# Kernel tuning notes

Measured on AMD Instinct MI355X. Metric: run time of the kernel, lower is better.

Reference implementation:

```python
import jax, jax.numpy as jnp
import numpy as np

V, E, U, B, T = 32000, 512, 1024, 32, 256


def setup_inputs() -> dict:
    key = jax.random.key(0)
    ks = jax.random.split(key, 6)
    rn = lambda k, shp, sc: jax.random.normal(k, shp, dtype=jnp.float32) * sc
    return {
        "x": jax.random.randint(ks[0], (B, T), 0, V, dtype=jnp.int32),
        "emb": rn(ks[1], (V, E), 0.02),
        "W_f": rn(ks[2], (E, 3 * U), 0.02),
        "U_f": rn(ks[3], (U, 3 * U), 0.02),
        "b_f": jnp.zeros((2, 3 * U), jnp.float32),
        "W_b": rn(ks[4], (E, 3 * U), 0.02),
        "U_b": rn(ks[5], (U, 3 * U), 0.02),
        "b_b": jnp.zeros((2, 3 * U), jnp.float32),
        "h0_f": jnp.zeros((B, U), jnp.float32),
        "h0_b": jnp.zeros((B, U), jnp.float32),
    }


def _gru_dir(x_tbe, h0, W, Ur, b):
    """Keras GRUCell (reset_after=True) over time. x_tbe: [T,B,E]."""
    # Precompute all input projections at once: [T,B,3U]
    xW = jnp.einsum('tbe,eg->tbg', x_tbe, W) + b[0]

    def step(h, xw):
        hU = h @ Ur + b[1]                      # [B,3U]
        xz, xr, xh = jnp.split(xw, 3, axis=-1)
        hz, hr, hn = jnp.split(hU, 3, axis=-1)
        z = jax.nn.sigmoid(xz + hz)
        r = jax.nn.sigmoid(xr + hr)
        n = jnp.tanh(xh + r * hn)
        h_new = z * h + (1.0 - z) * n
        return h_new, h_new

    hT, ys = jax.lax.scan(step, h0, xW)
    return ys, hT                                # ys: [T,B,U]


def reference(x, emb, W_f, U_f, b_f, W_b, U_b, b_b, h0_f, h0_b):
    xe = emb[x]                                  # [B,T,E] embedding lookup
    xt = jnp.transpose(xe, (1, 0, 2))            # [T,B,E]
    y_f, h_f = _gru_dir(xt, h0_f, W_f, U_f, b_f)
    y_b, h_b = _gru_dir(xt[::-1], h0_b, W_b, U_b, b_b)
    y_b = y_b[::-1]                              # re-align backward outputs in time
    y = jnp.concatenate([y_f, y_b], axis=-1)     # [T,B,2U]
    y = jnp.transpose(y, (1, 0, 2))              # [B,T,2U]
    return (y, h_f, h_b)
```

## Files before the change

kernel.cpp:

```cpp
#include <hip/hip_runtime.h>
#include <hip/hip_bf16.h>


typedef __attribute__((ext_vector_type(8))) short bf16x8;
typedef __attribute__((ext_vector_type(4))) float f32x4;

__device__ __forceinline__ f32x4 mfma_bf16(bf16x8 a, bf16x8 b, f32x4 c) {
  return __builtin_amdgcn_mfma_f32_16x16x32_bf16(a, b, c, 0, 0, 0);
}

__device__ __forceinline__ bf16x8 ld_b128(const __hip_bfloat16* p) {
  bf16x8 r; asm volatile("global_load_dwordx4 %0, %1, off" : "=v"(r) : "v"(p)); return r;
}
__device__ __forceinline__ bf16x8 ld_b128_dev(const unsigned* p) {
  bf16x8 r; asm volatile("global_load_dwordx4 %0, %1, off sc0 sc1" : "=v"(r) : "v"(p)); return r;
}
__device__ __forceinline__ unsigned ld_u32_pl(const void* p) {
  unsigned r; asm volatile("global_load_dword %0, %1, off" : "=v"(r) : "v"(p)); return r;
}
__device__ __forceinline__ unsigned ld_u32_dev(const unsigned* p) {
  unsigned r; asm volatile("global_load_dword %0, %1, off sc0 sc1" : "=v"(r) : "v"(p)); return r;
}
__device__ __forceinline__ void st_u32_dev(unsigned* p, unsigned v) {
  asm volatile("global_store_dword %0, %1, off sc0 sc1" :: "v"(p), "v"(v) : "memory");
}

__device__ __forceinline__ float bfsel(unsigned wd, int hi) {
  return __uint_as_float(hi ? (wd & 0xFFFF0000u) : (wd << 16));
}
__device__ __forceinline__ unsigned bfbits(float x) {
  return (unsigned)__builtin_bit_cast(unsigned short, __float2bfloat16(x));
}

#define WAITV(N) asm volatile("s_waitcnt vmcnt(" #N ")" ::: "memory")
#define SB0() __builtin_amdgcn_sched_barrier(0)


__global__ __launch_bounds__(256) void transpose_cast(const float* __restrict__ src,
                                                      __hip_bfloat16* __restrict__ dst,
                                                      int R, int C) {
  __shared__ float tile[32][33];
  const int tid = threadIdx.x;
  const int bc = blockIdx.x * 32;
  const int br = blockIdx.y * 32;
#pragma unroll
  for (int i = 0; i < 4; ++i) {
    int idx = tid + i * 256;
    int r = idx >> 5, c = idx & 31;
    tile[r][c] = src[(size_t)(br + r) * C + bc + c];
  }
  __syncthreads();
#pragma unroll
  for (int i = 0; i < 4; ++i) {
    int idx = tid + i * 256;
    int r = idx >> 5, c = idx & 31;
    dst[(size_t)(bc + r) * R + br + c] = __float2bfloat16(tile[c][r]);
  }
}

__global__ __launch_bounds__(256) void gather_embed(const int* __restrict__ x,
                                                    const float* __restrict__ emb,
                                                    __hip_bfloat16* __restrict__ A) {
  int ch = blockIdx.x * 256 + threadIdx.x;
  int row = ch >> 6, seg = ch & 63;
  int b = row & 31, t = row >> 5;
  int idx = x[b * 256 + t];
  const float* s = emb + (size_t)idx * 512 + seg * 8;
  float4 f0 = *(const float4*)(s);
  float4 f1 = *(const float4*)(s + 4);
  __hip_bfloat16 h[8];
  h[0] = __float2bfloat16(f0.x); h[1] = __float2bfloat16(f0.y);
  h[2] = __float2bfloat16(f0.z); h[3] = __float2bfloat16(f0.w);
  h[4] = __float2bfloat16(f1.x); h[5] = __float2bfloat16(f1.y);
  h[6] = __float2bfloat16(f1.z); h[7] = __float2bfloat16(f1.w);
  *(uint4*)(A + (size_t)row * 512 + seg * 8) = *(const uint4*)h;
}

__global__ __launch_bounds__(256) void init_h(const float* __restrict__ h0f,
                                              const float* __restrict__ h0b,
                                              unsigned* __restrict__ H,
                                              unsigned* __restrict__ FLG) {
  int i = blockIdx.x * 256 + threadIdx.x;
  int w = i >> 13, rem = i & 8191;
  int row = rem >> 9, p = rem & 511;
  const float* h0 = (w & 1) ? h0b : h0f;
  int b = (w >> 1) * 16 + row;
  float f0 = h0[b * 1024 + 2 * p];
  float f1 = h0[b * 1024 + 2 * p + 1];
  H[w * 16384 + row * 512 + p] = bfbits(f0) | (bfbits(f1) << 16);
  if (i < 8192) FLG[i] = 0u;
}

__global__ __launch_bounds__(256) void gemm_xw(const __hip_bfloat16* __restrict__ A,
                                               const __hip_bfloat16* __restrict__ B,
                                               __hip_bfloat16* __restrict__ C) {
  __shared__ char sm[2 * 128 * 80];
  const int tid = threadIdx.x;
  const int bn = blockIdx.x, bm = blockIdx.y;
  const int l = tid & 63, w = tid >> 6;
  const int wm = w & 1, wn = w >> 1;
  const int lr = l & 15, lk = l >> 4;
  f32x4 acc[4][4] = {};
  for (int k0 = 0; k0 < 512; k0 += 32) {
    __syncthreads();
#pragma unroll
    for (int i = 0; i < 2; ++i) {
      int ch = tid + i * 256;
      int row = ch >> 2, kq = ch & 3;
      uint4 va = *(const uint4*)(A + (size_t)(bm * 128 + row) * 512 + k0 + kq * 8);
      *(uint4*)(sm + row * 80 + kq * 16) = va;
      uint4 vb = *(const uint4*)(B + (size_t)(bn * 128 + row) * 512 + k0 + kq * 8);
      *(uint4*)(sm + 10240 + row * 80 + kq * 16) = vb;
    }
    __syncthreads();
    bf16x8 af[4], bfr[4];
#pragma unroll
    for (int m = 0; m < 4; ++m)
      af[m] = *(const bf16x8*)(sm + (wm * 64 + m * 16 + lr) * 80 + lk * 16);
#pragma unroll
    for (int n = 0; n < 4; ++n)
      bfr[n] = *(const bf16x8*)(sm + 10240 + (wn * 64 + n * 16 + lr) * 80 + lk * 16);
#pragma unroll
    for (int m = 0; m < 4; ++m)
#pragma unroll
      for (int n = 0; n < 4; ++n)
        acc[m][n] = mfma_bf16(af[m], bfr[n], acc[m][n]);
  }
#pragma unroll
  for (int m = 0; m < 4; ++m)
#pragma unroll
    for (int n = 0; n < 4; ++n)
#pragma unroll
      for (int v = 0; v < 4; ++v) {
        int row = bm * 128 + wm * 64 + m * 16 + lk * 4 + v;
        int col = bn * 128 + wn * 64 + n * 16 + lr;
        C[(size_t)row * 6144 + col] = __float2bfloat16(acc[m][n][v]);
      }
}

__global__ __launch_bounds__(512, 2) void gru_persist(
    const __hip_bfloat16* __restrict__ xW,
    const __hip_bfloat16* __restrict__ UT,
    const float* __restrict__ bias_f,
    const float* __restrict__ bias_b,
    const float* __restrict__ h0_f,
    const float* __restrict__ h0_b,
    unsigned* H,
    unsigned* FLG,
    float* __restrict__ out) {
  const int bi = blockIdx.x;
  const int w = bi & 3;
  const int r = bi >> 2;
  const int dir = w & 1, mh = w >> 1;
  const int tid = threadIdx.x;
  const int l = tid & 63, q = tid >> 6;
  const int lr = l & 15, lk = l >> 4;
  const int c0 = r * 32;

  __shared__ float xacc[8][6][16][20];

  bf16x8 ub[6][4];
#pragma unroll
  for (int g = 0; g < 3; ++g)
#pragma unroll
    for (int ch = 0; ch < 2; ++ch) {
      const __hip_bfloat16* Urow =
          UT + (size_t)(dir * 3072 + g * 1024 + c0 + ch * 16 + lr) * 1024 + q * 128 + lk * 8;
#pragma unroll
      for (int kc = 0; kc < 4; ++kc)
        ub[g * 2 + ch][kc] = ld_b128(Urow + kc * 32);
    }
  WAITV(0);
  SB0();

  const int crow = tid & 15;
  const int cp = tid >> 4;
  const int cb = mh * 16 + crow;
  const int cg = c0 + 2 * cp;
  float2 bz0, br0, bn0, bz1, br1, bn1, hp;
  if (tid < 256) {
    const float* bias = dir ? bias_b : bias_f;
    bz0 = *(const float2*)&bias[cg];
    br0 = *(const float2*)&bias[1024 + cg];
    bn0 = *(const float2*)&bias[2048 + cg];
    bz1 = *(const float2*)&bias[3072 + cg];
    br1 = *(const float2*)&bias[4096 + cg];
    bn1 = *(const float2*)&bias[5120 + cg];
    const float* h0 = dir ? h0_b : h0_f;
    hp = *(const float2*)&h0[(size_t)cb * 1024 + cg];
  }

  unsigned* Hw  = H + w * 16384;
  unsigned* FLw = FLG + w * 2048;
  const unsigned* flp = FLw + (16 * q + (l & 15)) * 16;
  unsigned* myflag = FLw + (r * 4 + q) * 16;

  for (int s = 0; s < 256; ++s) {
    const int par = s & 1;
    const int t = dir ? (255 - s) : s;

    unsigned xwz = 0, xwr = 0, xwn = 0;
    if (q < 4) {
      const __hip_bfloat16* xp = xW + (size_t)(t * 32 + cb) * 6144 + dir * 3072 + cg;
      xwz = ld_u32_pl(xp);
      xwr = ld_u32_pl(xp + 1024);
      xwn = ld_u32_pl(xp + 2048);
    }

    {
      const unsigned tg = (unsigned)s;
      for (;;) {
        unsigned f = ld_u32_dev(flp);
        WAITV(0);
        SB0();
        if (__all(f >= tg)) break;
        __builtin_amdgcn_s_sleep(1);
      }
    }

    const unsigned* hrow = Hw + par * 8192 + lr * 512 + q * 64 + lk * 4;
    bf16x8 hb[4];
#pragma unroll
    for (int kc = 0; kc < 4; ++kc)
      hb[kc] = ld_b128_dev(hrow + kc * 16);

    f32x4 acc[6] = {};
#define KSTEP(kc, n)                                                     \
    WAITV(n); SB0();                                                     \
    acc[0] = mfma_bf16(hb[kc], ub[0][kc], acc[0]);                       \
    acc[1] = mfma_bf16(hb[kc], ub[1][kc], acc[1]);                       \
    acc[2] = mfma_bf16(hb[kc], ub[2][kc], acc[2]);                       \
    acc[3] = mfma_bf16(hb[kc], ub[3][kc], acc[3]);                       \
    acc[4] = mfma_bf16(hb[kc], ub[4][kc], acc[4]);                       \
    acc[5] = mfma_bf16(hb[kc], ub[5][kc], acc[5]);
    KSTEP(0, 3) KSTEP(1, 2) KSTEP(2, 1) KSTEP(3, 0)
#undef KSTEP

    __syncthreads();

#pragma unroll
    for (int tile = 0; tile < 6; ++tile)
#pragma unroll
      for (int v = 0; v < 4; ++v)
        xacc[q][tile][lk * 4 + v][lr] = acc[tile][v];
    __syncthreads();

    if (tid < 256) {
      const int ch = cp >> 3;
      const int co = (2 * cp) & 15;
      float2 hz = {0.f, 0.f}, hr = {0.f, 0.f}, hn = {0.f, 0.f};
#pragma unroll
      for (int qq = 0; qq < 8; ++qq) {
        float2 a  = *(const float2*)&xacc[qq][ch][crow][co];
        float2 bq = *(const float2*)&xacc[qq][2 + ch][crow][co];
        float2 c  = *(const float2*)&xacc[qq][4 + ch][crow][co];
        hz.x += a.x;  hz.y += a.y;
        hr.x += bq.x; hr.y += bq.y;
        hn.x += c.x;  hn.y += c.y;
      }
      float hnew[2];
#pragma unroll
      for (int j = 0; j < 2; ++j) {
        const float hzj = j ? hz.y : hz.x, hrj = j ? hr.y : hr.x, hnj = j ? hn.y : hn.x;
        const float bz0j = j ? bz0.y : bz0.x, br0j = j ? br0.y : br0.x, bn0j = j ? bn0.y : bn0.x;
        const float bz1j = j ? bz1.y : bz1.x, br1j = j ? br1.y : br1.x, bn1j = j ? bn1.y : bn1.x;
        const float hpj = j ? hp.y : hp.x;
        const float z  = 1.f / (1.f + expf(-(bfsel(xwz, j) + bz0j + hzj + bz1j)));
        const float rr = 1.f / (1.f + expf(-(bfsel(xwr, j) + br0j + hrj + br1j)));
        const float n  = tanhf(bfsel(xwn, j) + bn0j + rr * (hnj + bn1j));
        hnew[j] = z * hpj + (1.f - z) * n;
      }
      hp.x = hnew[0]; hp.y = hnew[1];
      unsigned pk = bfbits(hnew[0]) | (bfbits(hnew[1]) << 16);
      st_u32_dev(Hw + (par ^ 1) * 8192 + crow * 512 + c0 / 2 + cp, pk);
      WAITV(0);
      if (l == 0) st_u32_dev(myflag, (unsigned)(s + 1));
      *(float2*)&out[((size_t)cb * 256 + t) * 2048 + dir * 1024 + cg] = *(float2*)hnew;
      if (s == 255)
        *(float2*)&out[16777216 + dir * 32768 + (size_t)cb * 1024 + cg] = *(float2*)hnew;
    }
  }
}


extern "C" void kernel_launch(void* const* d_in, const int* in_sizes, int n_in,
                              void* d_out, int out_size, void* d_ws, size_t ws_size,
                              hipStream_t stream) {
  const int*   x    = (const int*)d_in[0];
  const float* emb  = (const float*)d_in[1];
  const float* W_f  = (const float*)d_in[2];
  const float* U_f  = (const float*)d_in[3];
  const float* b_f  = (const float*)d_in[4];
  const float* W_b  = (const float*)d_in[5];
  const float* U_b  = (const float*)d_in[6];
  const float* b_b  = (const float*)d_in[7];
  const float* h0_f = (const float*)d_in[8];
  const float* h0_b = (const float*)d_in[9];
  float* out = (float*)d_out;
  char* ws = (char*)d_ws;

  const size_t SZ_A  = (size_t)8192 * 512 * 2;
  const size_t SZ_WT = (size_t)6144 * 512 * 2;
  const size_t SZ_UT = (size_t)6144 * 1024 * 2;
  const size_t SZ_XW = (size_t)8192 * 6144 * 2;
  const size_t SZ_H  = (size_t)4 * 16384 * 4;

  __hip_bfloat16* A   = (__hip_bfloat16*)(ws);
  __hip_bfloat16* WT  = (__hip_bfloat16*)(ws + SZ_A);
  __hip_bfloat16* UT  = (__hip_bfloat16*)(ws + SZ_A + SZ_WT);
  __hip_bfloat16* XW  = (__hip_bfloat16*)(ws + SZ_A + SZ_WT + SZ_UT);
  unsigned*       H   = (unsigned*)(ws + SZ_A + SZ_WT + SZ_UT + SZ_XW);
  unsigned*       FLG = (unsigned*)(ws + SZ_A + SZ_WT + SZ_UT + SZ_XW + SZ_H);

  transpose_cast<<<dim3(96, 16), 256, 0, stream>>>(W_f, WT, 512, 3072);
  transpose_cast<<<dim3(96, 16), 256, 0, stream>>>(W_b, WT + (size_t)3072 * 512, 512, 3072);
  transpose_cast<<<dim3(96, 32), 256, 0, stream>>>(U_f, UT, 1024, 3072);
  transpose_cast<<<dim3(96, 32), 256, 0, stream>>>(U_b, UT + (size_t)3072 * 1024, 1024, 3072);
  gather_embed<<<2048, 256, 0, stream>>>(x, emb, A);
  init_h<<<128, 256, 0, stream>>>(h0_f, h0_b, H, FLG);

  gemm_xw<<<dim3(48, 64), 256, 0, stream>>>(A, WT, XW);

  void* args[] = {(void*)&XW, (void*)&UT, (void*)&b_f, (void*)&b_b,
                  (void*)&h0_f, (void*)&h0_b, (void*)&H, (void*)&FLG, (void*)&out};
  hipLaunchCooperativeKernel((void*)gru_persist, dim3(128), dim3(512),
                             args, 0, stream);
}
```

Baseline: 1.133 ms.

## Embed step tags in hidden-state words to replace separate flag synchronization

```diff
diff --git a/kernel.cpp b/kernel.cpp
--- a/kernel.cpp
+++ b/kernel.cpp
@@ -4,6 +4,8 @@
 
 typedef __attribute__((ext_vector_type(8))) short bf16x8;
 typedef __attribute__((ext_vector_type(4))) float f32x4;
+typedef __attribute__((ext_vector_type(4))) unsigned u32x4;
+typedef __attribute__((ext_vector_type(2))) unsigned u32x2;
 
 __device__ __forceinline__ f32x4 mfma_bf16(bf16x8 a, bf16x8 b, f32x4 c) {
   return __builtin_amdgcn_mfma_f32_16x16x32_bf16(a, b, c, 0, 0, 0);
@@ -12,17 +14,14 @@
 __device__ __forceinline__ bf16x8 ld_b128(const __hip_bfloat16* p) {
   bf16x8 r; asm volatile("global_load_dwordx4 %0, %1, off" : "=v"(r) : "v"(p)); return r;
 }
-__device__ __forceinline__ bf16x8 ld_b128_dev(const unsigned* p) {
-  bf16x8 r; asm volatile("global_load_dwordx4 %0, %1, off sc0 sc1" : "=v"(r) : "v"(p)); return r;
+__device__ __forceinline__ u32x4 ld_v4_dev(const unsigned* p) {
+  u32x4 r; asm volatile("global_load_dwordx4 %0, %1, off sc0 sc1" : "=v"(r) : "v"(p)); return r;
 }
 __device__ __forceinline__ unsigned ld_u32_pl(const void* p) {
   unsigned r; asm volatile("global_load_dword %0, %1, off" : "=v"(r) : "v"(p)); return r;
 }
-__device__ __forceinline__ unsigned ld_u32_dev(const unsigned* p) {
-  unsigned r; asm volatile("global_load_dword %0, %1, off sc0 sc1" : "=v"(r) : "v"(p)); return r;
-}
-__device__ __forceinline__ void st_u32_dev(unsigned* p, unsigned v) {
-  asm volatile("global_store_dword %0, %1, off sc0 sc1" :: "v"(p), "v"(v) : "memory");
+__device__ __forceinline__ void st_v2_dev(unsigned* p, u32x2 v) {
+  asm volatile("global_store_dwordx2 %0, %1, off sc0 sc1" :: "v"(p), "v"(v) : "memory");
 }
 
 __device__ __forceinline__ float bfsel(unsigned wd, int hi) {
@@ -78,17 +77,19 @@
 
 __global__ __launch_bounds__(256) void init_h(const float* __restrict__ h0f,
                                               const float* __restrict__ h0b,
-                                              unsigned* __restrict__ H,
-                                              unsigned* __restrict__ FLG) {
+                                              unsigned* __restrict__ H) {
   int i = blockIdx.x * 256 + threadIdx.x;
-  int w = i >> 13, rem = i & 8191;
-  int row = rem >> 9, p = rem & 511;
-  const float* h0 = (w & 1) ? h0b : h0f;
-  int b = (w >> 1) * 16 + row;
-  float f0 = h0[b * 1024 + 2 * p];
-  float f1 = h0[b * 1024 + 2 * p + 1];
-  H[w * 16384 + row * 512 + p] = bfbits(f0) | (bfbits(f1) << 16);
-  if (i < 8192) FLG[i] = 0u;
+  int w = i >> 15, rem = i & 32767;
+  int par = rem >> 14, rem2 = rem & 16383;
+  int row = rem2 >> 10, col = rem2 & 1023;
+  unsigned v;
+  if (par == 0) {
+    const float* h0 = (w & 1) ? h0b : h0f;
+    v = bfbits(h0[((w >> 1) * 16 + row) * 1024 + col]) << 16;
+  } else {
+    v = 0xFFFFu;
+  }
+  H[i] = v;
 }
 
 __global__ __launch_bounds__(256) void gemm_xw(const __hip_bfloat16* __restrict__ A,
@@ -146,7 +147,6 @@
     const float* __restrict__ h0_f,
     const float* __restrict__ h0_b,
     unsigned* H,
-    unsigned* FLG,
     float* __restrict__ out) {
   const int bi = blockIdx.x;
   const int w = bi & 3;
@@ -190,10 +190,7 @@
     hp = *(const float2*)&h0[(size_t)cb * 1024 + cg];
   }
 
-  unsigned* Hw  = H + w * 16384;
-  unsigned* FLw = FLG + w * 2048;
-  const unsigned* flp = FLw + (16 * q + (l & 15)) * 16;
-  unsigned* myflag = FLw + (r * 4 + q) * 16;
+  unsigned* Hw = H + w * 32768;
 
   for (int s = 0; s < 256; ++s) {
     const int par = s & 1;
@@ -207,34 +204,41 @@
       xwn = ld_u32_pl(xp + 2048);
     }
 
-    {
-      const unsigned tg = (unsigned)s;
-      for (;;) {
-        unsigned f = ld_u32_dev(flp);
-        WAITV(0);
-        SB0();
-        if (__all(f >= tg)) break;
-        __builtin_amdgcn_s_sleep(1);
+    const unsigned* hrow = Hw + par * 16384 + lr * 1024 + q * 128 + lk * 8;
+    const unsigned tg = (unsigned)s;
+    u32x4 ta[8];
+    for (;;) {
+#pragma unroll
+      for (int kc = 0; kc < 4; ++kc) {
+        ta[2 * kc]     = ld_v4_dev(hrow + kc * 32);
+        ta[2 * kc + 1] = ld_v4_dev(hrow + kc * 32 + 4);
       }
-    }
-
-    const unsigned* hrow = Hw + par * 8192 + lr * 512 + q * 64 + lk * 4;
-    bf16x8 hb[4];
-#pragma unroll
-    for (int kc = 0; kc < 4; ++kc)
-      hb[kc] = ld_b128_dev(hrow + kc * 16);
+      WAITV(0);
+      SB0();
+      unsigned bad = 0;
+#pragma unroll
+      for (int i = 0; i < 8; ++i)
+        bad |= (ta[i][0] ^ tg) | (ta[i][1] ^ tg) | (ta[i][2] ^ tg) | (ta[i][3] ^ tg);
+      if (__all((bad & 0xFFFFu) == 0)) break;
+      __builtin_amdgcn_s_sleep(1);
+    }
 
     f32x4 acc[6] = {};
-#define KSTEP(kc, n)                                                     \
-    WAITV(n); SB0();                                                     \
-    acc[0] = mfma_bf16(hb[kc], ub[0][kc], acc[0]);                       \
-    acc[1] = mfma_bf16(hb[kc], ub[1][kc], acc[1]);                       \
-    acc[2] = mfma_bf16(hb[kc], ub[2][kc], acc[2]);                       \
-    acc[3] = mfma_bf16(hb[kc], ub[3][kc], acc[3]);                       \
-    acc[4] = mfma_bf16(hb[kc], ub[4][kc], acc[4]);                       \
-    acc[5] = mfma_bf16(hb[kc], ub[5][kc], acc[5]);
-    KSTEP(0, 3) KSTEP(1, 2) KSTEP(2, 1) KSTEP(3, 0)
-#undef KSTEP
+#pragma unroll
+    for (int kc = 0; kc < 4; ++kc) {
+      u32x4 pk;
+      pk[0] = (ta[2 * kc][0] >> 16)     | (ta[2 * kc][1] & 0xFFFF0000u);
+      pk[1] = (ta[2 * kc][2] >> 16)     | (ta[2 * kc][3] & 0xFFFF0000u);
+      pk[2] = (ta[2 * kc + 1][0] >> 16) | (ta[2 * kc + 1][1] & 0xFFFF0000u);
+      pk[3] = (ta[2 * kc + 1][2] >> 16) | (ta[2 * kc + 1][3] & 0xFFFF0000u);
+      bf16x8 hb = __builtin_bit_cast(bf16x8, pk);
+      acc[0] = mfma_bf16(hb, ub[0][kc], acc[0]);
+      acc[1] = mfma_bf16(hb, ub[1][kc], acc[1]);
+      acc[2] = mfma_bf16(hb, ub[2][kc], acc[2]);
+      acc[3] = mfma_bf16(hb, ub[3][kc], acc[3]);
+      acc[4] = mfma_bf16(hb, ub[4][kc], acc[4]);
+      acc[5] = mfma_bf16(hb, ub[5][kc], acc[5]);
+    }
 
     __syncthreads();
 
@@ -271,10 +275,10 @@
         hnew[j] = z * hpj + (1.f - z) * n;
       }
       hp.x = hnew[0]; hp.y = hnew[1];
-      unsigned pk = bfbits(hnew[0]) | (bfbits(hnew[1]) << 16);
-      st_u32_dev(Hw + (par ^ 1) * 8192 + crow * 512 + c0 / 2 + cp, pk);
-      WAITV(0);
-      if (l == 0) st_u32_dev(myflag, (unsigned)(s + 1));
+      u32x2 pk2;
+      pk2[0] = (bfbits(hnew[0]) << 16) | (unsigned)(s + 1);
+      pk2[1] = (bfbits(hnew[1]) << 16) | (unsigned)(s + 1);
+      st_v2_dev(Hw + (par ^ 1) * 16384 + crow * 1024 + cg, pk2);
       *(float2*)&out[((size_t)cb * 256 + t) * 2048 + dir * 1024 + cg] = *(float2*)hnew;
       if (s == 255)
         *(float2*)&out[16777216 + dir * 32768 + (size_t)cb * 1024 + cg] = *(float2*)hnew;
@@ -303,26 +307,24 @@
   const size_t SZ_WT = (size_t)6144 * 512 * 2;
   const size_t SZ_UT = (size_t)6144 * 1024 * 2;
   const size_t SZ_XW = (size_t)8192 * 6144 * 2;
-  const size_t SZ_H  = (size_t)4 * 16384 * 4;
 
   __hip_bfloat16* A   = (__hip_bfloat16*)(ws);
   __hip_bfloat16* WT  = (__hip_bfloat16*)(ws + SZ_A);
   __hip_bfloat16* UT  = (__hip_bfloat16*)(ws + SZ_A + SZ_WT);
   __hip_bfloat16* XW  = (__hip_bfloat16*)(ws + SZ_A + SZ_WT + SZ_UT);
   unsigned*       H   = (unsigned*)(ws + SZ_A + SZ_WT + SZ_UT + SZ_XW);
-  unsigned*       FLG = (unsigned*)(ws + SZ_A + SZ_WT + SZ_UT + SZ_XW + SZ_H);
 
   transpose_cast<<<dim3(96, 16), 256, 0, stream>>>(W_f, WT, 512, 3072);
   transpose_cast<<<dim3(96, 16), 256, 0, stream>>>(W_b, WT + (size_t)3072 * 512, 512, 3072);
   transpose_cast<<<dim3(96, 32), 256, 0, stream>>>(U_f, UT, 1024, 3072);
   transpose_cast<<<dim3(96, 32), 256, 0, stream>>>(U_b, UT + (size_t)3072 * 1024, 1024, 3072);
   gather_embed<<<2048, 256, 0, stream>>>(x, emb, A);
-  init_h<<<128, 256, 0, stream>>>(h0_f, h0_b, H, FLG);
+  init_h<<<512, 256, 0, stream>>>(h0_f, h0_b, H);
 
   gemm_xw<<<dim3(48, 64), 256, 0, stream>>>(A, WT, XW);
 
   void* args[] = {(void*)&XW, (void*)&UT, (void*)&b_f, (void*)&b_b,
-                  (void*)&h0_f, (void*)&h0_b, (void*)&H, (void*)&FLG, (void*)&out};
+                  (void*)&h0_f, (void*)&h0_b, (void*)&H, (void*)&out};
   hipLaunchCooperativeKernel((void*)gru_persist, dim3(128), dim3(512),
                              args, 0, stream);
 }
```

After: 1.886 ms. 66.4% more time.
